# Performance work log

Measured on AMD Instinct MI355X. Metric: run time of the kernel, lower is better.

## Reference

```python
import jax, jax.numpy as jnp
import numpy as np

N_NODES = 100000
N_EDGES = 1600000
D = 64
K = 5


def setup_inputs() -> dict:
    key = jax.random.key(0)
    k1, k2, k3, k4 = jax.random.split(key, 4)
    x = jax.random.normal(k1, (N_NODES, D), dtype=jnp.float32)
    # random edges, guaranteed no self-loops (offset in [1, N-1])
    src = jax.random.randint(k2, (N_EDGES,), 0, N_NODES)
    off = jax.random.randint(k3, (N_EDGES,), 1, N_NODES)
    dst = (src + off) % N_NODES
    edge_index = jnp.stack([src, dst], axis=0)  # [2, E], row 0 = source j, row 1 = target i
    kW, kb = jax.random.split(k4)
    W = jax.random.normal(kW, (K, D, D), dtype=jnp.float32) * (1.0 / np.sqrt(D))
    b = jnp.zeros((D,), dtype=jnp.float32)
    return {"x": x, "edge_index": edge_index, "W": W, "b": b}


def reference(x, edge_index, W, b):
    """ChebConv (normalization='sym', lambda_max=2.0) as in PyG GnBlock.

    Scaled Laplacian L_hat = (2/lambda_max) * (I - D^-1/2 A D^-1/2) - I
    with lambda_max=2 has zero diagonal, so propagate(h) = sum over edges
    (j->i) of norm_e * h[j] with norm_e = -dis[j]*dis[i].
    """
    src, dst = edge_index[0], edge_index[1]
    n = x.shape[0]
    # degree over source nodes (PyG get_laplacian scatters edge_weight=1 over row)
    deg = jax.ops.segment_sum(jnp.ones_like(src, dtype=x.dtype), src, num_segments=n)
    dis = jnp.where(deg > 0, jax.lax.rsqrt(jnp.maximum(deg, 1e-30)), 0.0)
    norm = -dis[src] * dis[dst]  # [E]

    def prop(h):
        # message: norm_e * h[src], aggregated at dst
        return jax.ops.segment_sum(norm[:, None] * h[src], dst, num_segments=n)

    Tx0 = x
    out = Tx0 @ W[0]
    Tx1 = prop(x)
    out = out + Tx1 @ W[1]
    for k in range(2, W.shape[0]):
        Tx2 = 2.0 * prop(Tx1) - Tx0
        out = out + Tx2 @ W[k]
        Tx0, Tx1 = Tx1, Tx2
    return out + b
```

## Files before the change

### kernel.cpp

```cpp
#include <hip/hip_runtime.h>

#define DD 64
#define NPB 16
#define NBKMAX 128
#define CAPB 20480
#define EPB 8
#define EPT 20
#define ASTR 72

typedef _Float16 f16x8 __attribute__((ext_vector_type(8)));
typedef float f32x4 __attribute__((ext_vector_type(4)));

__global__ __launch_bounds__(1024) void histA_kernel(
        const int* __restrict__ src, const int* __restrict__ dst,
        int* __restrict__ gbcnt, unsigned int* __restrict__ bktbuf,
        unsigned char* __restrict__ srcp, int NR,
        int E, int nbk) {
    extern __shared__ unsigned int ldsH[];
    __shared__ int lcnt[NBKMAX];
    __shared__ int lbase[NBKMAX];
    int nw = NR >> 2;
    int t = threadIdx.x;
    for (int i = t; i < nw; i += 1024) ldsH[i] = 0u;
    if (t < NBKMAX) lcnt[t] = 0;
    __syncthreads();
    int base = blockIdx.x * (EPB * 1024);
    unsigned int ent[EPB];
    int rk[EPB];
    int bk[EPB];
    #pragma unroll
    for (int k = 0; k < EPB; ++k) {
        int e = base + t + k * 1024;
        bk[k] = -1;
        if (e < E) {
            int s = __builtin_nontemporal_load(src + e);
            int d = __builtin_nontemporal_load(dst + e);
            atomicAdd(&ldsH[s >> 2], 1u << ((unsigned int)(s & 3) * 8u));
            int b = d >> 10;
            ent[k] = ((unsigned int)s << 10) | (unsigned int)(d & 1023);
            rk[k] = atomicAdd(&lcnt[b], 1);
            bk[k] = b;
        }
    }
    __syncthreads();
    if (t < nbk) lbase[t] = atomicAdd(&gbcnt[t], lcnt[t]);
    __syncthreads();
    #pragma unroll
    for (int k = 0; k < EPB; ++k) {
        if (bk[k] >= 0) {
            int pos = lbase[bk[k]] + rk[k];
            if (pos < CAPB)
                __builtin_nontemporal_store(ent[k],
                    bktbuf + (size_t)bk[k] * CAPB + pos);
        }
    }
    unsigned int* outp = reinterpret_cast<unsigned int*>(srcp + (size_t)blockIdx.x * NR);
    for (int i = t; i < nw; i += 1024) outp[i] = ldsH[i];
}

__global__ void disred_kernel(const unsigned char* __restrict__ srcp,
                              float* __restrict__ dis, int N, int NR, int na) {
    int g = blockIdx.x * 256 + threadIdx.x;
    if (g < N) {
        int degv = 0;
        for (int i = 0; i < na; ++i) degv += srcp[(size_t)i * NR + g];
        dis[g] = (degv > 0) ? rsqrtf((float)degv) : 0.0f;
    }
}

__global__ __launch_bounds__(1024) void csrB_kernel(
        const unsigned int* __restrict__ bktbuf, const int* __restrict__ gbcnt,
        int* __restrict__ rowptr, int* __restrict__ adjS,
        int N, int nbk, int E) {
    __shared__ int ncnt[1024];
    __shared__ int tmp[1024];
    __shared__ int adjstage[CAPB];
    __shared__ int bbase_s;
    int b = blockIdx.x;
    int t = threadIdx.x;
    if (t == 0) {
        int acc = 0;
        for (int i = 0; i < b; ++i) acc += gbcnt[i];
        bbase_s = acc;
    }
    ncnt[t] = 0;
    __syncthreads();
    int total = min(gbcnt[b], CAPB);
    int bbase = bbase_s;
    const unsigned int* bp = bktbuf + (size_t)b * CAPB;
    unsigned int sv[EPT];
    int rk[EPT];
    int dl[EPT];
    #pragma unroll
    for (int k = 0; k < EPT; ++k) {
        int i = t + k * 1024;
        dl[k] = -1;
        if (i < total) {
            unsigned int v = bp[i];
            sv[k] = v >> 10;
            int d = (int)(v & 1023u);
            dl[k] = d;
            rk[k] = atomicAdd(&ncnt[d], 1);
        }
    }
    __syncthreads();
    int v = ncnt[t];
    tmp[t] = v;
    __syncthreads();
    for (int off = 1; off < 1024; off <<= 1) {
        int a = (t >= off) ? tmp[t - off] : 0;
        __syncthreads();
        tmp[t] += a;
        __syncthreads();
    }
    int excl = tmp[t] - v;
    int node = b * 1024 + t;
    if (node < N) rowptr[node] = bbase + excl;
    if (b == nbk - 1 && t == 1023) rowptr[N] = E;
    __syncthreads();
    ncnt[t] = excl;
    __syncthreads();
    #pragma unroll
    for (int k = 0; k < EPT; ++k)
        if (dl[k] >= 0) adjstage[ncnt[dl[k]] + rk[k]] = (int)sv[k];
    __syncthreads();
    for (int i = t; i < total; i += 1024)
        adjS[bbase + i] = adjstage[i];
}

__global__ void cvt_kernel(const float* __restrict__ x, const float* __restrict__ dis,
                           _Float16* __restrict__ p0, long long n8) {
    long long i = (long long)blockIdx.x * blockDim.x + threadIdx.x;
    if (i < n8) {
        int node = (int)(i >> 3);
        float dv = dis[node];
        float f = (dv > 0.f) ? dv : 1.0f;
        const float4* x4 = reinterpret_cast<const float4*>(x);
        float4 a = x4[i * 2], b = x4[i * 2 + 1];
        f16x8 h;
        h[0] = (_Float16)(f * a.x); h[1] = (_Float16)(f * a.y);
        h[2] = (_Float16)(f * a.z); h[3] = (_Float16)(f * a.w);
        h[4] = (_Float16)(f * b.x); h[5] = (_Float16)(f * b.y);
        h[6] = (_Float16)(f * b.z); h[7] = (_Float16)(f * b.w);
        reinterpret_cast<f16x8*>(p0)[i] = h;
    }
}

__global__ void wcvt_kernel(const float* __restrict__ W, _Float16* __restrict__ Wh,
                            int nfrag) {
    int idx = blockIdx.x * blockDim.x + threadIdx.x;
    if (idx >= nfrag) return;
    int lane = idx & 63;
    int ct = (idx >> 6) & 3;
    int kt = (idx >> 8) & 1;
    int k = idx >> 9;
    int r0 = kt * 32 + (lane >> 4) * 8;
    int c = ct * 16 + (lane & 15);
    f16x8 h;
    #pragma unroll
    for (int i = 0; i < 8; ++i)
        h[i] = (_Float16)W[(size_t)k * DD * DD + (size_t)(r0 + i) * DD + c];
    reinterpret_cast<f16x8*>(Wh)[idx] = h;
}

__global__ __launch_bounds__(256, 8) void prop_kernel(
        const int* __restrict__ rowptr, const int* __restrict__ adjS,
        const float* __restrict__ dis,
        const _Float16* __restrict__ h, const _Float16* t0,
        _Float16* __restrict__ pout, float scale, int N) {
    int t = threadIdx.x;
    int nl = t >> 6, lane = t & 63;
    int q = lane & 7;
    int s = (lane >> 3) & 1;
    int ng = lane >> 4;
    int node = blockIdx.x * NPB + nl * 4 + ng;
    bool valid = node < N;
    const f16x8* h8 = reinterpret_cast<const f16x8*>(h);

    int beg = 0, end = 0;
    if (valid) { beg = rowptr[node]; end = rowptr[node + 1]; }

    float acc[8];
    #pragma unroll
    for (int i = 0; i < 8; ++i) acc[i] = 0.f;

    int j = beg + s;
    int e0 = (j < end) ? adjS[j] : 0;
    int e1 = (j + 2 < end) ? adjS[j + 2] : 0;
    int e2 = (j + 4 < end) ? adjS[j + 4] : 0;
    int e3 = (j + 6 < end) ? adjS[j + 6] : 0;
    float m0 = (j < end) ? 1.f : 0.f;
    float m1 = (j + 2 < end) ? 1.f : 0.f;
    float m2 = (j + 4 < end) ? 1.f : 0.f;
    float m3 = (j + 6 < end) ? 1.f : 0.f;
    while (j < end) {
        int jn = j + 8;
        int n0 = (jn < end) ? adjS[jn] : 0;
        int n1 = (jn + 2 < end) ? adjS[jn + 2] : 0;
        int n2 = (jn + 4 < end) ? adjS[jn + 4] : 0;
        int n3 = (jn + 6 < end) ? adjS[jn + 6] : 0;
        float nm0 = (jn < end) ? 1.f : 0.f;
        float nm1 = (jn + 2 < end) ? 1.f : 0.f;
        float nm2 = (jn + 4 < end) ? 1.f : 0.f;
        float nm3 = (jn + 6 < end) ? 1.f : 0.f;
        f16x8 g0 = h8[(size_t)e0 * 8 + q];
        f16x8 g1 = h8[(size_t)e1 * 8 + q];
        f16x8 g2 = h8[(size_t)e2 * 8 + q];
        f16x8 g3 = h8[(size_t)e3 * 8 + q];
        #pragma unroll
        for (int i = 0; i < 8; ++i) {
            acc[i] += m0 * (float)g0[i] + m1 * (float)g1[i];
            acc[i] += m2 * (float)g2[i] + m3 * (float)g3[i];
        }
        e0 = n0; e1 = n1; e2 = n2; e3 = n3;
        m0 = nm0; m1 = nm1; m2 = nm2; m3 = nm3;
        j = jn;
    }
    #pragma unroll
    for (int i = 0; i < 8; ++i) acc[i] += __shfl_xor(acc[i], 8, 64);

    if (s == 0 && valid) {
        float dv = dis[node];
        float cf = scale * dv * dv;
        size_t base = (size_t)node * DD + q * 8;
        f16x8 vh;
        if (t0) {
            f16x8 t0v = __builtin_nontemporal_load(
                reinterpret_cast<const f16x8*>(t0 + base));
            #pragma unroll
            for (int i = 0; i < 8; ++i)
                vh[i] = (_Float16)(cf * acc[i] - (float)t0v[i]);
        } else {
            #pragma unroll
            for (int i = 0; i < 8; ++i) vh[i] = (_Float16)(cf * acc[i]);
        }
        *reinterpret_cast<f16x8*>(pout + base) = vh;
    }
}

static __device__ __forceinline__ f16x8 afrag(const _Float16* __restrict__ P,
                                              int node, int kt, int lk) {
    return *reinterpret_cast<const f16x8*>(P + (size_t)node * DD + kt * 32 + lk * 8);
}

__global__ __launch_bounds__(256, 6) void prop_last_kernel(
        const int* __restrict__ rowptr, const int* __restrict__ adjS,
        const float* __restrict__ dis,
        const _Float16* __restrict__ h , const _Float16* __restrict__ t0 ,
        const _Float16* __restrict__ P0, const _Float16* __restrict__ P1,
        const _Float16* __restrict__ Wh, const float* __restrict__ bias,
        float* __restrict__ out, int N) {
    __shared__ _Float16 A_lds[NPB][ASTR];
    int t = threadIdx.x;
    int nl = t >> 6, lane = t & 63;
    int q = lane & 7;
    int s = (lane >> 3) & 1;
    int ng = lane >> 4;
    int nb0 = blockIdx.x * NPB;
    int node = nb0 + nl * 4 + ng;
    bool valid = node < N;
    const f16x8* h8 = reinterpret_cast<const f16x8*>(h);

    int beg = 0, end = 0;
    if (valid) { beg = rowptr[node]; end = rowptr[node + 1]; }

    float acc[8];
    #pragma unroll
    for (int i = 0; i < 8; ++i) acc[i] = 0.f;

    int j = beg + s;
    int e0 = (j < end) ? adjS[j] : 0;
    int e1 = (j + 2 < end) ? adjS[j + 2] : 0;
    int e2 = (j + 4 < end) ? adjS[j + 4] : 0;
    int e3 = (j + 6 < end) ? adjS[j + 6] : 0;
    float m0 = (j < end) ? 1.f : 0.f;
    float m1 = (j + 2 < end) ? 1.f : 0.f;
    float m2 = (j + 4 < end) ? 1.f : 0.f;
    float m3 = (j + 6 < end) ? 1.f : 0.f;
    while (j < end) {
        int jn = j + 8;
        int n0 = (jn < end) ? adjS[jn] : 0;
        int n1 = (jn + 2 < end) ? adjS[jn + 2] : 0;
        int n2 = (jn + 4 < end) ? adjS[jn + 4] : 0;
        int n3 = (jn + 6 < end) ? adjS[jn + 6] : 0;
        float nm0 = (jn < end) ? 1.f : 0.f;
        float nm1 = (jn + 2 < end) ? 1.f : 0.f;
        float nm2 = (jn + 4 < end) ? 1.f : 0.f;
        float nm3 = (jn + 6 < end) ? 1.f : 0.f;
        f16x8 g0 = h8[(size_t)e0 * 8 + q];
        f16x8 g1 = h8[(size_t)e1 * 8 + q];
        f16x8 g2 = h8[(size_t)e2 * 8 + q];
        f16x8 g3 = h8[(size_t)e3 * 8 + q];
        #pragma unroll
        for (int i = 0; i < 8; ++i) {
            acc[i] += m0 * (float)g0[i] + m1 * (float)g1[i];
            acc[i] += m2 * (float)g2[i] + m3 * (float)g3[i];
        }
        e0 = n0; e1 = n1; e2 = n2; e3 = n3;
        m0 = nm0; m1 = nm1; m2 = nm2; m3 = nm3;
        j = jn;
    }
    #pragma unroll
    for (int i = 0; i < 8; ++i) acc[i] += __shfl_xor(acc[i], 8, 64);

    if (s == 0 && valid) {
        float dv = dis[node];
        float cf = -2.0f * dv * dv;
        size_t base = (size_t)node * DD + q * 8;
        f16x8 t0v = __builtin_nontemporal_load(
            reinterpret_cast<const f16x8*>(t0 + base));
        f16x8 vh;
        #pragma unroll
        for (int i = 0; i < 8; ++i)
            vh[i] = (_Float16)(cf * acc[i] - (float)t0v[i]);
        *reinterpret_cast<f16x8*>(&A_lds[nl * 4 + ng][q * 8]) = vh;
    }
    __syncthreads();

    int ct = nl, lr = lane & 15, lk = lane >> 4;
    const f16x8* Wh8 = reinterpret_cast<const f16x8*>(Wh);
    f16x8 bf[5][2];
    #pragma unroll
    for (int k = 0; k < 5; ++k)
        #pragma unroll
        for (int kt = 0; kt < 2; ++kt)
            bf[k][kt] = Wh8[((k * 2 + kt) * 4 + ct) * 64 + lane];
    int gn = min(nb0 + lr, N - 1);
    f32x4 d = {0.f, 0.f, 0.f, 0.f};
    #pragma unroll
    for (int kt = 0; kt < 2; ++kt) {
        f16x8 a4 = *reinterpret_cast<const f16x8*>(&A_lds[lr][kt * 32 + lk * 8]);
        d = __builtin_amdgcn_mfma_f32_16x16x32_f16(afrag(P0, gn, kt, lk), bf[0][kt], d, 0, 0, 0);
        d = __builtin_amdgcn_mfma_f32_16x16x32_f16(afrag(P1, gn, kt, lk), bf[1][kt], d, 0, 0, 0);
        d = __builtin_amdgcn_mfma_f32_16x16x32_f16(afrag(t0, gn, kt, lk), bf[2][kt], d, 0, 0, 0);
        d = __builtin_amdgcn_mfma_f32_16x16x32_f16(afrag(h,  gn, kt, lk), bf[3][kt], d, 0, 0, 0);
        d = __builtin_amdgcn_mfma_f32_16x16x32_f16(a4, bf[4][kt], d, 0, 0, 0);
    }
    int nvb = min(NPB, N - nb0);
    int col = ct * 16 + lr;
    float bv = bias[col];
    #pragma unroll
    for (int r = 0; r < 4; ++r) {
        int row = lk * 4 + r;
        if (row < nvb) {
            float dv = dis[nb0 + row];
            float invd = (dv > 0.f) ? 1.f / dv : 1.f;
            long long o = (long long)(nb0 + row) * DD + col;
            __builtin_nontemporal_store(bv + invd * d[r], out + o);
        }
    }
}

__global__ __launch_bounds__(256, 8) void gemm2_kernel(
        const _Float16* __restrict__ P0, const _Float16* __restrict__ P1,
        const float* __restrict__ dis,
        const float* __restrict__ W0, const float* __restrict__ W1,
        const float* __restrict__ bias, float* __restrict__ out, int N) {
    int t = threadIdx.x;
    int nl = t >> 6, lane = t & 63;
    int ct = nl, lr = lane & 15, lk = lane >> 4;
    f16x8 bf0[2], bf1[2];
    #pragma unroll
    for (int kt = 0; kt < 2; ++kt)
        #pragma unroll
        for (int i = 0; i < 8; ++i) {
            int r = kt * 32 + lk * 8 + i;
            bf0[kt][i] = (_Float16)W0[r * DD + ct * 16 + lr];
            bf1[kt][i] = (_Float16)W1[r * DD + ct * 16 + lr];
        }
    int nb0 = blockIdx.x * NPB;
    int node = min(nb0 + lr, N - 1);
    f32x4 d = {0.f, 0.f, 0.f, 0.f};
    #pragma unroll
    for (int kt = 0; kt < 2; ++kt) {
        d = __builtin_amdgcn_mfma_f32_16x16x32_f16(afrag(P0, node, kt, lk), bf0[kt], d, 0, 0, 0);
        d = __builtin_amdgcn_mfma_f32_16x16x32_f16(afrag(P1, node, kt, lk), bf1[kt], d, 0, 0, 0);
    }
    int nvb = min(NPB, N - nb0);
    int col = ct * 16 + lr;
    float bv = bias[col];
    #pragma unroll
    for (int r = 0; r < 4; ++r) {
        int row = lk * 4 + r;
        if (row < nvb) {
            float dv = dis[nb0 + row];
            float invd = (dv > 0.f) ? 1.f / dv : 1.f;
            long long o = (long long)(nb0 + row) * DD + col;
            out[o] = bv + invd * d[r];
        }
    }
}

__global__ __launch_bounds__(256, 8) void gemm1_kernel(
        const _Float16* __restrict__ P, const float* __restrict__ dis,
        const float* __restrict__ Wk, float* __restrict__ out, int N) {
    int t = threadIdx.x;
    int nl = t >> 6, lane = t & 63;
    int ct = nl, lr = lane & 15, lk = lane >> 4;
    f16x8 bf[2];
    #pragma unroll
    for (int kt = 0; kt < 2; ++kt)
        #pragma unroll
        for (int i = 0; i < 8; ++i) {
            int r = kt * 32 + lk * 8 + i;
            bf[kt][i] = (_Float16)Wk[r * DD + ct * 16 + lr];
        }
    int nb0 = blockIdx.x * NPB;
    int node = min(nb0 + lr, N - 1);
    f32x4 d = {0.f, 0.f, 0.f, 0.f};
    #pragma unroll
    for (int kt = 0; kt < 2; ++kt)
        d = __builtin_amdgcn_mfma_f32_16x16x32_f16(afrag(P, node, kt, lk), bf[kt], d, 0, 0, 0);
    int nvb = min(NPB, N - nb0);
    int col = ct * 16 + lr;
    #pragma unroll
    for (int r = 0; r < 4; ++r) {
        int row = lk * 4 + r;
        if (row < nvb) {
            float dv = dis[nb0 + row];
            float invd = (dv > 0.f) ? 1.f / dv : 1.f;
            long long o = (long long)(nb0 + row) * DD + col;
            out[o] = out[o] + invd * d[r];
        }
    }
}

extern "C" void kernel_launch(void* const* d_in, const int* in_sizes, int n_in,
                              void* d_out, int out_size, void* d_ws, size_t ws_size,
                              hipStream_t stream) {
    const float* x  = (const float*)d_in[0];
    const int*   ei = (const int*)d_in[1];
    const float* W  = (const float*)d_in[2];
    const float* b  = (const float*)d_in[3];
    float* out = (float*)d_out;

    const int N = in_sizes[0] / DD;
    const int E = in_sizes[1] / 2;
    const int K = in_sizes[2] / (DD * DD);
    const long long ND = (long long)N * DD;
    const int NR = ((N + 3) / 4) * 4;
    const int nbk = (N + 1023) >> 10;
    const int na = (E + EPB * 1024 - 1) / (EPB * 1024);

    const int* src = ei;
    const int* dst = ei + E;

    size_t off = 0;
    char* base = (char*)d_ws;
    auto alloc = [&](size_t bytes) {
        char* p = base + off;
        off = (off + bytes + 63) & ~(size_t)63;
        return p;
    };
    float* dis = (float*)alloc((size_t)N * 4);
    int* rowptr = (int*)alloc((size_t)(N + 1) * 4);
    _Float16* Wh = (_Float16*)alloc((size_t)5 * 2 * 4 * 64 * 8 * 2);
    int* gbcnt = (int*)alloc((size_t)NBKMAX * 4);
    char* ovl = alloc((size_t)na * NR + (size_t)NBKMAX * CAPB * 4);
    unsigned char* srcp = (unsigned char*)ovl;
    unsigned int* bktbuf = (unsigned int*)(ovl + (size_t)na * NR);
    int* adjS = (int*)alloc((size_t)E * 4);
    _Float16* P0 = (_Float16*)alloc((size_t)ND * 2);
    _Float16* P1 = (_Float16*)alloc((size_t)ND * 2);
    _Float16* P3 = (_Float16*)alloc((size_t)ND * 2);
    _Float16* P2 = (_Float16*)ovl;

    (void)hipMemsetAsync(gbcnt, 0, (size_t)NBKMAX * 4, stream);

    histA_kernel<<<na, 1024, (size_t)NR, stream>>>(src, dst, gbcnt, bktbuf,
                                                   srcp, NR, E, nbk);
    disred_kernel<<<(N + 255) / 256, 256, 0, stream>>>(srcp, dis, N, NR, na);
    csrB_kernel<<<nbk, 1024, 0, stream>>>(bktbuf, gbcnt, rowptr, adjS, N, nbk, E);

    const long long n8 = ND / 8;
    cvt_kernel<<<(int)((n8 + 255) / 256), 256, 0, stream>>>(x, dis, P0, n8);
    if (K == 5) {
        const int nfrag = 5 * 2 * 4 * 64;
        wcvt_kernel<<<(nfrag + 255) / 256, 256, 0, stream>>>(W, Wh, nfrag);
    }

    const int pgrid = (N + NPB - 1) / NPB;
    const int Wsz = DD * DD;

    if (K == 5) {
        prop_kernel<<<pgrid, 256, 0, stream>>>(rowptr, adjS, dis, P0,
                                               (const _Float16*)0, P1, -1.0f, N);
        prop_kernel<<<pgrid, 256, 0, stream>>>(rowptr, adjS, dis, P1, P0, P2, -2.0f, N);
        prop_kernel<<<pgrid, 256, 0, stream>>>(rowptr, adjS, dis, P2, P1, P3, -2.0f, N);
        prop_last_kernel<<<pgrid, 256, 0, stream>>>(rowptr, adjS, dis, P3, P2,
                                                    P0, P1, Wh, b, out, N);
    } else {
        prop_kernel<<<pgrid, 256, 0, stream>>>(rowptr, adjS, dis, P0,
                                               (const _Float16*)0, P1, -1.0f, N);
        gemm2_kernel<<<pgrid, 256, 0, stream>>>(P0, P1, dis, W, W + Wsz, b, out, N);
        _Float16* t0 = P0;
        _Float16* h  = P1;
        _Float16* fr = P2;
        for (int k = 2; k < K; ++k) {
            prop_kernel<<<pgrid, 256, 0, stream>>>(rowptr, adjS, dis, h, t0, fr, -2.0f, N);
            gemm1_kernel<<<pgrid, 256, 0, stream>>>(fr, dis, W + (long long)k * Wsz,
                                                    out, N);
            _Float16* nfree = t0;
            t0 = h; h = fr; fr = nfree;
        }
    }
}
```

Baseline: 343.3 us.

## Split source-degree histogram out of bucketing kernel and stage bucket counts in LDS

Moves the per-block byte histogram of source degrees into its own kernel, histS, which runs a fixed grid of 256 blocks, each covering a contiguous edge slice. The bucketing kernel histA no longer needs about 100KB of dynamic LDS, so more of its blocks can be resident at once. csrB now copies the global bucket counts into shared memory before computing its prefix base, replacing serial global loads. The cost is an extra kernel launch, a second read of the source array, and a larger partial-histogram buffer for disred to reduce.

```diff
diff --git a/kernel.cpp b/kernel.cpp
--- a/kernel.cpp
+++ b/kernel.cpp
@@ -2,6 +2,7 @@
 
 #define DD 64
 #define NPB 16
+#define NBS 256
 #define NBKMAX 128
 #define CAPB 20480
 #define EPB 8
@@ -11,17 +12,43 @@
 typedef _Float16 f16x8 __attribute__((ext_vector_type(8)));
 typedef float f32x4 __attribute__((ext_vector_type(4)));
 
+__global__ __launch_bounds__(1024) void histS_kernel(
+        const int* __restrict__ src, unsigned char* __restrict__ srcp,
+        int N, int NR, int E, int slice) {
+    extern __shared__ unsigned int ldsH[];
+    int nw = NR >> 2;
+    int t = threadIdx.x;
+    for (int i = t; i < nw; i += 1024) ldsH[i] = 0u;
+    __syncthreads();
+    int base = blockIdx.x * slice;
+    int end = min(base + slice, E);
+    for (int e = base + t; e < end; e += 1024) {
+        int s = __builtin_nontemporal_load(src + e);
+        atomicAdd(&ldsH[s >> 2], 1u << ((unsigned int)(s & 3) * 8u));
+    }
+    __syncthreads();
+    unsigned int* outp = reinterpret_cast<unsigned int*>(srcp + (size_t)blockIdx.x * NR);
+    for (int i = t; i < nw; i += 1024) outp[i] = ldsH[i];
+}
+
+__global__ void disred_kernel(const unsigned char* __restrict__ srcp,
+                              float* __restrict__ dis, int N, int NR) {
+    int g = blockIdx.x * 256 + threadIdx.x;
+    if (g < N) {
+        int degv = 0;
+        #pragma unroll 8
+        for (int i = 0; i < NBS; ++i) degv += srcp[(size_t)i * NR + g];
+        dis[g] = (degv > 0) ? rsqrtf((float)degv) : 0.0f;
+    }
+}
+
 __global__ __launch_bounds__(1024) void histA_kernel(
         const int* __restrict__ src, const int* __restrict__ dst,
         int* __restrict__ gbcnt, unsigned int* __restrict__ bktbuf,
-        unsigned char* __restrict__ srcp, int NR,
         int E, int nbk) {
-    extern __shared__ unsigned int ldsH[];
     __shared__ int lcnt[NBKMAX];
     __shared__ int lbase[NBKMAX];
-    int nw = NR >> 2;
-    int t = threadIdx.x;
-    for (int i = t; i < nw; i += 1024) ldsH[i] = 0u;
+    int t = threadIdx.x;
     if (t < NBKMAX) lcnt[t] = 0;
     __syncthreads();
     int base = blockIdx.x * (EPB * 1024);
@@ -35,7 +62,6 @@
         if (e < E) {
             int s = __builtin_nontemporal_load(src + e);
             int d = __builtin_nontemporal_load(dst + e);
-            atomicAdd(&ldsH[s >> 2], 1u << ((unsigned int)(s & 3) * 8u));
             int b = d >> 10;
             ent[k] = ((unsigned int)s << 10) | (unsigned int)(d & 1023);
             rk[k] = atomicAdd(&lcnt[b], 1);
@@ -53,18 +79,6 @@
                 __builtin_nontemporal_store(ent[k],
                     bktbuf + (size_t)bk[k] * CAPB + pos);
         }
-    }
-    unsigned int* outp = reinterpret_cast<unsigned int*>(srcp + (size_t)blockIdx.x * NR);
-    for (int i = t; i < nw; i += 1024) outp[i] = ldsH[i];
-}
-
-__global__ void disred_kernel(const unsigned char* __restrict__ srcp,
-                              float* __restrict__ dis, int N, int NR, int na) {
-    int g = blockIdx.x * 256 + threadIdx.x;
-    if (g < N) {
-        int degv = 0;
-        for (int i = 0; i < na; ++i) degv += srcp[(size_t)i * NR + g];
-        dis[g] = (degv > 0) ? rsqrtf((float)degv) : 0.0f;
     }
 }
 
@@ -75,17 +89,20 @@
     __shared__ int ncnt[1024];
     __shared__ int tmp[1024];
     __shared__ int adjstage[CAPB];
+    __shared__ int gb[NBKMAX];
     __shared__ int bbase_s;
     int b = blockIdx.x;
     int t = threadIdx.x;
+    if (t < NBKMAX) gb[t] = (t < nbk) ? gbcnt[t] : 0;
+    ncnt[t] = 0;
+    __syncthreads();
     if (t == 0) {
         int acc = 0;
-        for (int i = 0; i < b; ++i) acc += gbcnt[i];
+        for (int i = 0; i < b; ++i) acc += gb[i];
         bbase_s = acc;
     }
-    ncnt[t] = 0;
-    __syncthreads();
-    int total = min(gbcnt[b], CAPB);
+    __syncthreads();
+    int total = min(gb[b], CAPB);
     int bbase = bbase_s;
     const unsigned int* bp = bktbuf + (size_t)b * CAPB;
     unsigned int sv[EPT];
@@ -440,7 +457,6 @@
     const long long ND = (long long)N * DD;
     const int NR = ((N + 3) / 4) * 4;
     const int nbk = (N + 1023) >> 10;
-    const int na = (E + EPB * 1024 - 1) / (EPB * 1024);
 
     const int* src = ei;
     const int* dst = ei + E;
@@ -456,9 +472,9 @@
     int* rowptr = (int*)alloc((size_t)(N + 1) * 4);
     _Float16* Wh = (_Float16*)alloc((size_t)5 * 2 * 4 * 64 * 8 * 2);
     int* gbcnt = (int*)alloc((size_t)NBKMAX * 4);
-    char* ovl = alloc((size_t)na * NR + (size_t)NBKMAX * CAPB * 4);
+    char* ovl = alloc((size_t)NBS * NR + (size_t)NBKMAX * CAPB * 4);
     unsigned char* srcp = (unsigned char*)ovl;
-    unsigned int* bktbuf = (unsigned int*)(ovl + (size_t)na * NR);
+    unsigned int* bktbuf = (unsigned int*)(ovl + (size_t)NBS * NR);
     int* adjS = (int*)alloc((size_t)E * 4);
     _Float16* P0 = (_Float16*)alloc((size_t)ND * 2);
     _Float16* P1 = (_Float16*)alloc((size_t)ND * 2);
@@ -467,9 +483,12 @@
 
     (void)hipMemsetAsync(gbcnt, 0, (size_t)NBKMAX * 4, stream);
 
-    histA_kernel<<<na, 1024, (size_t)NR, stream>>>(src, dst, gbcnt, bktbuf,
-                                                   srcp, NR, E, nbk);
-    disred_kernel<<<(N + 255) / 256, 256, 0, stream>>>(srcp, dis, N, NR, na);
+    const int sliceS = (E + NBS - 1) / NBS;
+    histS_kernel<<<NBS, 1024, (size_t)NR, stream>>>(src, srcp, N, NR, E, sliceS);
+    disred_kernel<<<(N + 255) / 256, 256, 0, stream>>>(srcp, dis, N, NR);
+
+    const int na = (E + EPB * 1024 - 1) / (EPB * 1024);
+    histA_kernel<<<na, 1024, 0, stream>>>(src, dst, gbcnt, bktbuf, E, nbk);
     csrB_kernel<<<nbk, 1024, 0, stream>>>(bktbuf, gbcnt, rowptr, adjS, N, nbk, E);
 
     const long long n8 = ND / 8;
```

Result: faster. 315.5 us (-8.1%).
